# Optimization experiments

Measured on AMD Instinct MI355X. Metric: run time of the kernel, lower is better.

## Reference

```python
import jax, jax.numpy as jnp
import numpy as np

TEMPERATURE = 0.1
SINGLE_POS = False
EPS = 1e-8  # torch CosineSimilarity eps
B, D = 8192, 128
N_DATA = 100000


def setup_inputs() -> dict:
    key = jax.random.key(0)
    k1, k2, k3, k4 = jax.random.split(key, 4)
    features = jax.random.normal(k1, (B, D), dtype=jnp.float32)
    data_ix = jax.random.randint(k2, (B,), 0, N_DATA, dtype=jnp.int64)
    targets_t = jax.random.randint(k3, (N_DATA,), 0, 2, dtype=jnp.int64)
    targets_p = jax.random.randint(k4, (N_DATA,), 0, 2, dtype=jnp.int64)
    return {"features": features, "data_ix": data_ix,
            "targets_t": targets_t, "targets_p": targets_p}


def reference(features, data_ix, targets_t, targets_p):
    tt = targets_t[data_ix]  # [B]
    tp = targets_p[data_ix]  # [B]

    # cosine similarity matrix [B, B] (torch CosineSimilarity semantics)
    norms = jnp.linalg.norm(features, axis=1)  # [B]
    dots = features @ features.T               # [B, B]
    sim = dots / jnp.maximum(norms[:, None] * norms[None, :], EPS)
    logits = sim / TEMPERATURE                 # log(exp(sim/T)) == sim/T
    exp_sim = jnp.exp(logits)

    # pos: same true label, different predicted label; neg: reversed
    same_t = tt[:, None] == tt[None, :]
    same_p = tp[:, None] == tp[None, :]
    pos_mask = same_t & ~same_p   # excludes self automatically
    neg_mask = ~same_t & same_p

    pos_cnt = pos_mask.sum(axis=1)  # [B]
    neg_cnt = neg_mask.sum(axis=1)  # [B]

    exp_pos_sum = jnp.sum(jnp.where(pos_mask, exp_sim, 0.0), axis=1)  # [B]
    exp_neg_sum = jnp.sum(jnp.where(neg_mask, exp_sim, 0.0), axis=1)  # [B]

    if SINGLE_POS:
        # per-pair denominator: log(exp_neg_sum + exp_pos_ij)
        log_denom = jnp.log(exp_neg_sum[:, None] + exp_sim)  # [B, B]
        log_probs_sum = jnp.sum(jnp.where(pos_mask, logits - log_denom, 0.0), axis=1)
    else:
        log_denom = jnp.log(exp_neg_sum + exp_pos_sum)  # [B]
        log_probs_sum = jnp.sum(jnp.where(pos_mask, logits - log_denom[:, None], 0.0), axis=1)

    valid = (pos_cnt > 0) & (neg_cnt > 0)
    mean_log_probs = jnp.where(valid,
                               log_probs_sum / jnp.maximum(pos_cnt, 1).astype(logits.dtype),
                               0.0)
    loss = -jnp.sum(mean_log_probs) / features.shape[0]
    return loss
```

## Files before the change

### kernel.cpp

```cpp
#include <hip/hip_runtime.h>


#define NB 8192
#define ND 128
#define NIB 64
#define JS 16
#define TEMP_INV 10.0f
#define LOG2E 1.4426950408889634f
#define EXPK (TEMP_INV * LOG2E)

typedef __attribute__((ext_vector_type(8))) short short8;
typedef __attribute__((ext_vector_type(4))) float f32x4;

#define OFF_G    0
#define OFF_CLS  (NB * ND * 2)
#define OFF_CNT  (OFF_CLS + NB)
#define OFF_EPP  (OFF_CNT + 64)
#define OFF_ENP  (OFF_EPP + NB * 4 * JS)
#define OFF_LSP  (OFF_ENP + NB * 4 * JS)
#define OFF_CO   OFF_EPP
#define OFF_RL   (OFF_EPP + NB)

__device__ __forceinline__ unsigned short f2bf(float x) {
    unsigned int u = __float_as_uint(x);
    unsigned int r = (u + 0x7FFFu + ((u >> 16) & 1u)) >> 16;
    return (unsigned short)r;
}

__device__ __forceinline__ float fast_exp2(float x) {
#if __has_builtin(__builtin_amdgcn_exp2f)
    return __builtin_amdgcn_exp2f(x);
#else
    return exp2f(x);
#endif
}

__global__ __launch_bounds__(256) void classify_kernel(
    const int* __restrict__ dix, const int* __restrict__ tt, const int* __restrict__ tp,
    unsigned char* __restrict__ clsO, unsigned short* __restrict__ rlocal,
    int* __restrict__ cntP, float* __restrict__ out)
{
    __shared__ int lh[4];
    const int h = blockIdx.x, tid = threadIdx.x;
    if (tid < 4) lh[tid] = 0;
    __syncthreads();
    #pragma unroll
    for (int k = 0; k < 8; ++k) {
        const int row = h * 2048 + k * 256 + tid;
        const int ix  = dix[row];
        const int c   = ((tt[ix] & 1) << 1) | (tp[ix] & 1);
        clsO[row] = (unsigned char)c;
        rlocal[row] = (unsigned short)atomicAdd(&lh[c], 1);
    }
    if (h == 0 && tid == 0) *out = 0.0f;
    __syncthreads();
    if (tid < 4) cntP[h * 4 + tid] = lh[tid];
}

__global__ __launch_bounds__(256) void normscatter_kernel(
    const float* __restrict__ F, const unsigned char* __restrict__ clsO,
    const unsigned short* __restrict__ rlocal, const int* __restrict__ cntP,
    unsigned short* __restrict__ G, unsigned char* __restrict__ clsS)
{
    const int row  = blockIdx.x * 4 + (threadIdx.x >> 6);
    const int lane = threadIdx.x & 63;
    const int c = clsO[row];
    const int h = row >> 11;
    int base = (int)rlocal[row];
    #pragma unroll
    for (int cc = 0; cc < 3; ++cc)
        if (cc < c) base += cntP[cc] + cntP[4 + cc] + cntP[8 + cc] + cntP[12 + cc];
    #pragma unroll
    for (int hh = 0; hh < 3; ++hh)
        if (hh < h) base += cntP[hh * 4 + c];

    const float2 v = *(const float2*)(F + row * ND + lane * 2);
    float ss = v.x * v.x + v.y * v.y;
    #pragma unroll
    for (int m = 1; m < 64; m <<= 1) ss += __shfl_xor(ss, m, 64);
    const float inv = rsqrtf(fmaxf(ss, 1e-24f));
    ushort2 st; st.x = f2bf(v.x * inv); st.y = f2bf(v.y * inv);
    *(ushort2*)(G + base * ND + lane * 2) = st;
    if (lane == 0) clsS[base] = (unsigned char)c;
}

template<bool DOP, bool DON>
__device__ __forceinline__ void seg_tiles(
    const unsigned short* __restrict__ G,
    const short8 (&A)[2][4], unsigned int rcLo, unsigned int rcHi, int s,
    float (&Ep)[8], float (&En)[8], float (&Ls)[8],
    int cs, int ce, int t0, int t1, int l16, int q)
{
    const int s1 = s ^ 1, s2 = s ^ 2;
    float wp[8], wn[8];
    #pragma unroll
    for (int r = 0; r < 4; ++r) {
        const int cLo = (rcLo >> (8 * r)) & 0xff;
        const int cHi = (rcHi >> (8 * r)) & 0xff;
        if (DOP) { wp[r] = (cLo == s1) ? 1.f : 0.f; wp[4 + r] = (cHi == s1) ? 1.f : 0.f; }
        if (DON) { wn[r] = (cLo == s2) ? 1.f : 0.f; wn[4 + r] = (cHi == s2) ? 1.f : 0.f; }
    }
    for (int t = t0; t < t1; ++t) {
        const int j0 = cs + (t << 4);
        int jc = j0 + l16;
        jc = (jc < NB - 1) ? jc : (NB - 1);
        const unsigned short* gj = G + jc * ND + q * 8;
        short8 Bf[4];
        #pragma unroll
        for (int c = 0; c < 4; ++c) Bf[c] = *(const short8*)(gj + c * 32);
        f32x4 acc0 = {0.f, 0.f, 0.f, 0.f}, acc1 = {0.f, 0.f, 0.f, 0.f};
        #pragma unroll
        for (int c = 0; c < 4; ++c)
            acc0 = __builtin_amdgcn_mfma_f32_16x16x32_bf16(A[0][c], Bf[c], acc0, 0, 0, 0);
        #pragma unroll
        for (int c = 0; c < 4; ++c)
            acc1 = __builtin_amdgcn_mfma_f32_16x16x32_bf16(A[1][c], Bf[c], acc1, 0, 0, 0);
        if (j0 + 16 <= ce) {
            #pragma unroll
            for (int r = 0; r < 4; ++r) {
                const float sv0 = acc0[r], sv1 = acc1[r];
                const float e0 = fast_exp2(sv0 * EXPK);
                const float e1 = fast_exp2(sv1 * EXPK);
                if (DOP) {
                    Ep[r]     = fmaf(wp[r],     e0,  Ep[r]);
                    Ls[r]     = fmaf(wp[r],     sv0, Ls[r]);
                    Ep[4 + r] = fmaf(wp[4 + r], e1,  Ep[4 + r]);
                    Ls[4 + r] = fmaf(wp[4 + r], sv1, Ls[4 + r]);
                }
                if (DON) {
                    En[r]     = fmaf(wn[r],     e0, En[r]);
                    En[4 + r] = fmaf(wn[4 + r], e1, En[4 + r]);
                }
            }
        } else {
            const float vm = ((j0 + l16) < ce) ? 1.f : 0.f;
            #pragma unroll
            for (int r = 0; r < 4; ++r) {
                const float sv0 = acc0[r] * vm, sv1 = acc1[r] * vm;
                const float e0 = fast_exp2(sv0 * EXPK) * vm;
                const float e1 = fast_exp2(sv1 * EXPK) * vm;
                if (DOP) {
                    Ep[r]     = fmaf(wp[r],     e0,  Ep[r]);
                    Ls[r]     = fmaf(wp[r],     sv0, Ls[r]);
                    Ep[4 + r] = fmaf(wp[4 + r], e1,  Ep[4 + r]);
                    Ls[4 + r] = fmaf(wp[4 + r], sv1, Ls[4 + r]);
                }
                if (DON) {
                    En[r]     = fmaf(wn[r],     e0, En[r]);
                    En[4 + r] = fmaf(wn[4 + r], e1, En[4 + r]);
                }
            }
        }
    }
}

__global__ __launch_bounds__(256, 4) void sim_kernel(
    const unsigned short* __restrict__ G, const unsigned char* __restrict__ clsS,
    const int* __restrict__ cntP,
    float* __restrict__ EpP, float* __restrict__ EnP, float* __restrict__ LsP)
{
    const int ib = blockIdx.x & (NIB - 1);
    const int jb = blockIdx.x >> 6;
    const int wave = threadIdx.x >> 6, lane = threadIdx.x & 63;
    const int q = lane >> 4, l16 = lane & 15;
    const int ri = ib * 128 + wave * 32;

    short8 A[2][4];
    #pragma unroll
    for (int t = 0; t < 2; ++t)
        #pragma unroll
        for (int c = 0; c < 4; ++c)
            A[t][c] = *(const short8*)(G + (ri + 16 * t + l16) * ND + c * 32 + q * 8);

    const unsigned int rcLo = *(const unsigned int*)(clsS + ri + 4 * q);
    const unsigned int rcHi = *(const unsigned int*)(clsS + ri + 16 + 4 * q);
    const int wF = clsS[ri], wL = clsS[ri + 31];

    float Ep[8], En[8], Ls[8];
    #pragma unroll
    for (int i = 0; i < 8; ++i) { Ep[i] = 0.f; En[i] = 0.f; Ls[i] = 0.f; }

    int cs = 0;
    #pragma unroll 1
    for (int s = 0; s < 4; ++s) {
        const int len = cntP[s] + cntP[4 + s] + cntP[8 + s] + cntP[12 + s];
        const int ce = cs + len;
        const int s1 = s ^ 1, s2 = s ^ 2;
        const bool aP = (s1 >= wF) && (s1 <= wL);
        const bool aN = (s2 >= wF) && (s2 <= wL);
        if (aP || aN) {
            const int nt = (len + 15) >> 4;
            const int t0 = (jb * nt) >> 4;
            const int t1 = ((jb + 1) * nt) >> 4;
            if (aP && aN) seg_tiles<true,  true >(G, A, rcLo, rcHi, s, Ep, En, Ls, cs, ce, t0, t1, l16, q);
            else if (aP)  seg_tiles<true,  false>(G, A, rcLo, rcHi, s, Ep, En, Ls, cs, ce, t0, t1, l16, q);
            else          seg_tiles<false, true >(G, A, rcLo, rcHi, s, Ep, En, Ls, cs, ce, t0, t1, l16, q);
        }
        cs = ce;
    }

    #pragma unroll
    for (int m = 1; m < 16; m <<= 1)
        #pragma unroll
        for (int i = 0; i < 8; ++i) {
            Ep[i] += __shfl_xor(Ep[i], m, 64);
            En[i] += __shfl_xor(En[i], m, 64);
            Ls[i] += __shfl_xor(Ls[i], m, 64);
        }
    if (l16 == 0) {
        #pragma unroll
        for (int t = 0; t < 2; ++t)
            #pragma unroll
            for (int r = 0; r < 4; ++r) {
                const int row = ri + 16 * t + 4 * q + r;
                const int i = t * 4 + r;
                EpP[jb * NB + row] = Ep[i];
                EnP[jb * NB + row] = En[i];
                LsP[jb * NB + row] = Ls[i];
            }
    }
}

__global__ __launch_bounds__(256) void finalize_kernel(
    const float* __restrict__ EpP, const float* __restrict__ EnP,
    const float* __restrict__ LsP, const unsigned char* __restrict__ clsS,
    const int* __restrict__ cntP, float* __restrict__ out)
{
    const int i = blockIdx.x * 256 + threadIdx.x;
    const int tot0 = cntP[0] + cntP[4] + cntP[8]  + cntP[12];
    const int tot1 = cntP[1] + cntP[5] + cntP[9]  + cntP[13];
    const int tot2 = cntP[2] + cntP[6] + cntP[10] + cntP[14];
    const int tot3 = cntP[3] + cntP[7] + cntP[11] + cntP[15];
    const int c = clsS[i];
    const int pc = c ^ 1, nc = c ^ 2;
    const int pcnt = (pc == 0) ? tot0 : (pc == 1) ? tot1 : (pc == 2) ? tot2 : tot3;
    const int ncnt = (nc == 0) ? tot0 : (nc == 1) ? tot1 : (nc == 2) ? tot2 : tot3;
    float ep = 0.f, en = 0.f, ls = 0.f;
    #pragma unroll
    for (int jb = 0; jb < JS; ++jb) {
        ep += EpP[jb * NB + i];
        en += EnP[jb * NB + i];
        ls += LsP[jb * NB + i];
    }
    float contrib = 0.0f;
    if (pcnt > 0 && ncnt > 0) {
        const float ld = logf(ep + en);
        contrib = -(TEMP_INV * ls - (float)pcnt * ld) / ((float)pcnt * (float)NB);
    }
    #pragma unroll
    for (int m = 1; m < 64; m <<= 1) contrib += __shfl_xor(contrib, m, 64);
    __shared__ float wsum[4];
    if ((threadIdx.x & 63) == 0) wsum[threadIdx.x >> 6] = contrib;
    __syncthreads();
    if (threadIdx.x == 0)
        atomicAdd(out, wsum[0] + wsum[1] + wsum[2] + wsum[3]);
}

extern "C" void kernel_launch(void* const* d_in, const int* in_sizes, int n_in,
                              void* d_out, int out_size, void* d_ws, size_t ws_size,
                              hipStream_t stream) {
    const float* F = (const float*)d_in[0];
    const int* dix = (const int*)d_in[1];
    const int* tt  = (const int*)d_in[2];
    const int* tp  = (const int*)d_in[3];
    float* out = (float*)d_out;

    char* ws = (char*)d_ws;
    unsigned short* G   = (unsigned short*)(ws + OFF_G);
    unsigned char* clsS = (unsigned char*)(ws + OFF_CLS);
    int* cntP           = (int*)(ws + OFF_CNT);
    float* EpP          = (float*)(ws + OFF_EPP);
    float* EnP          = (float*)(ws + OFF_ENP);
    float* LsP          = (float*)(ws + OFF_LSP);
    unsigned char* clsO = (unsigned char*)(ws + OFF_CO);
    unsigned short* rl  = (unsigned short*)(ws + OFF_RL);

    classify_kernel<<<4, 256, 0, stream>>>(dix, tt, tp, clsO, rl, cntP, out);
    normscatter_kernel<<<2048, 256, 0, stream>>>(F, clsO, rl, cntP, G, clsS);
    sim_kernel<<<NIB * JS, 256, 0, stream>>>(G, clsS, cntP, EpP, EnP, LsP);
    finalize_kernel<<<NB / 256, 256, 0, stream>>>(EpP, EnP, LsP, clsS, cntP, out);
}
```

Measured before the change: 119.7 us.

## Stage B tiles cooperatively in shared memory with register-prefetched double buffering

Each 16-row B tile was previously loaded from global memory separately by every wave. Now the four waves load it together into a double-buffered LDS tile, and the next tile is prefetched into registers, so global traffic per block drops about fourfold and loads overlap with MFMA work. In exchange the activity test moves from per-wave to per-block class ranges, extra barriers are added per tile, and waves with no work still have to join the barrier loop.

```diff
diff --git a/kernel.cpp b/kernel.cpp
--- a/kernel.cpp
+++ b/kernel.cpp
@@ -11,6 +11,7 @@
 
 typedef __attribute__((ext_vector_type(8))) short short8;
 typedef __attribute__((ext_vector_type(4))) float f32x4;
+typedef __attribute__((ext_vector_type(4))) unsigned int u32x4;
 
 #define OFF_G    0
 #define OFF_CLS  (NB * ND * 2)
@@ -84,86 +85,19 @@
     if (lane == 0) clsS[base] = (unsigned char)c;
 }
 
-template<bool DOP, bool DON>
-__device__ __forceinline__ void seg_tiles(
-    const unsigned short* __restrict__ G,
-    const short8 (&A)[2][4], unsigned int rcLo, unsigned int rcHi, int s,
-    float (&Ep)[8], float (&En)[8], float (&Ls)[8],
-    int cs, int ce, int t0, int t1, int l16, int q)
-{
-    const int s1 = s ^ 1, s2 = s ^ 2;
-    float wp[8], wn[8];
-    #pragma unroll
-    for (int r = 0; r < 4; ++r) {
-        const int cLo = (rcLo >> (8 * r)) & 0xff;
-        const int cHi = (rcHi >> (8 * r)) & 0xff;
-        if (DOP) { wp[r] = (cLo == s1) ? 1.f : 0.f; wp[4 + r] = (cHi == s1) ? 1.f : 0.f; }
-        if (DON) { wn[r] = (cLo == s2) ? 1.f : 0.f; wn[4 + r] = (cHi == s2) ? 1.f : 0.f; }
-    }
-    for (int t = t0; t < t1; ++t) {
-        const int j0 = cs + (t << 4);
-        int jc = j0 + l16;
-        jc = (jc < NB - 1) ? jc : (NB - 1);
-        const unsigned short* gj = G + jc * ND + q * 8;
-        short8 Bf[4];
-        #pragma unroll
-        for (int c = 0; c < 4; ++c) Bf[c] = *(const short8*)(gj + c * 32);
-        f32x4 acc0 = {0.f, 0.f, 0.f, 0.f}, acc1 = {0.f, 0.f, 0.f, 0.f};
-        #pragma unroll
-        for (int c = 0; c < 4; ++c)
-            acc0 = __builtin_amdgcn_mfma_f32_16x16x32_bf16(A[0][c], Bf[c], acc0, 0, 0, 0);
-        #pragma unroll
-        for (int c = 0; c < 4; ++c)
-            acc1 = __builtin_amdgcn_mfma_f32_16x16x32_bf16(A[1][c], Bf[c], acc1, 0, 0, 0);
-        if (j0 + 16 <= ce) {
-            #pragma unroll
-            for (int r = 0; r < 4; ++r) {
-                const float sv0 = acc0[r], sv1 = acc1[r];
-                const float e0 = fast_exp2(sv0 * EXPK);
-                const float e1 = fast_exp2(sv1 * EXPK);
-                if (DOP) {
-                    Ep[r]     = fmaf(wp[r],     e0,  Ep[r]);
-                    Ls[r]     = fmaf(wp[r],     sv0, Ls[r]);
-                    Ep[4 + r] = fmaf(wp[4 + r], e1,  Ep[4 + r]);
-                    Ls[4 + r] = fmaf(wp[4 + r], sv1, Ls[4 + r]);
-                }
-                if (DON) {
-                    En[r]     = fmaf(wn[r],     e0, En[r]);
-                    En[4 + r] = fmaf(wn[4 + r], e1, En[4 + r]);
-                }
-            }
-        } else {
-            const float vm = ((j0 + l16) < ce) ? 1.f : 0.f;
-            #pragma unroll
-            for (int r = 0; r < 4; ++r) {
-                const float sv0 = acc0[r] * vm, sv1 = acc1[r] * vm;
-                const float e0 = fast_exp2(sv0 * EXPK) * vm;
-                const float e1 = fast_exp2(sv1 * EXPK) * vm;
-                if (DOP) {
-                    Ep[r]     = fmaf(wp[r],     e0,  Ep[r]);
-                    Ls[r]     = fmaf(wp[r],     sv0, Ls[r]);
-                    Ep[4 + r] = fmaf(wp[4 + r], e1,  Ep[4 + r]);
-                    Ls[4 + r] = fmaf(wp[4 + r], sv1, Ls[4 + r]);
-                }
-                if (DON) {
-                    En[r]     = fmaf(wn[r],     e0, En[r]);
-                    En[4 + r] = fmaf(wn[4 + r], e1, En[4 + r]);
-                }
-            }
-        }
-    }
-}
-
 __global__ __launch_bounds__(256, 4) void sim_kernel(
     const unsigned short* __restrict__ G, const unsigned char* __restrict__ clsS,
     const int* __restrict__ cntP,
     float* __restrict__ EpP, float* __restrict__ EnP, float* __restrict__ LsP)
 {
+    __shared__ __align__(16) unsigned short Bt[2][16][136];
+
     const int ib = blockIdx.x & (NIB - 1);
     const int jb = blockIdx.x >> 6;
     const int wave = threadIdx.x >> 6, lane = threadIdx.x & 63;
     const int q = lane >> 4, l16 = lane & 15;
     const int ri = ib * 128 + wave * 32;
+    const int wr = wave << 2;
 
     short8 A[2][4];
     #pragma unroll
@@ -175,10 +109,13 @@
     const unsigned int rcLo = *(const unsigned int*)(clsS + ri + 4 * q);
     const unsigned int rcHi = *(const unsigned int*)(clsS + ri + 16 + 4 * q);
     const int wF = clsS[ri], wL = clsS[ri + 31];
+    const int bF = clsS[ib * 128], bL = clsS[ib * 128 + 127];
 
     float Ep[8], En[8], Ls[8];
     #pragma unroll
     for (int i = 0; i < 8; ++i) { Ep[i] = 0.f; En[i] = 0.f; Ls[i] = 0.f; }
+
+    const u32x4* G4 = (const u32x4*)G;
 
     int cs = 0;
     #pragma unroll 1
@@ -186,15 +123,107 @@
         const int len = cntP[s] + cntP[4 + s] + cntP[8 + s] + cntP[12 + s];
         const int ce = cs + len;
         const int s1 = s ^ 1, s2 = s ^ 2;
-        const bool aP = (s1 >= wF) && (s1 <= wL);
-        const bool aN = (s2 >= wF) && (s2 <= wL);
+        const bool aP = (s1 >= bF) && (s1 <= bL);
+        const bool aN = (s2 >= bF) && (s2 <= bL);
         if (aP || aN) {
             const int nt = (len + 15) >> 4;
             const int t0 = (jb * nt) >> 4;
             const int t1 = ((jb + 1) * nt) >> 4;
-            if (aP && aN) seg_tiles<true,  true >(G, A, rcLo, rcHi, s, Ep, En, Ls, cs, ce, t0, t1, l16, q);
-            else if (aP)  seg_tiles<true,  false>(G, A, rcLo, rcHi, s, Ep, En, Ls, cs, ce, t0, t1, l16, q);
-            else          seg_tiles<false, true >(G, A, rcLo, rcHi, s, Ep, En, Ls, cs, ce, t0, t1, l16, q);
+            if (t0 < t1) {
+                float wp[8], wn[8];
+                #pragma unroll
+                for (int r = 0; r < 4; ++r) {
+                    const int cLo = (rcLo >> (8 * r)) & 0xff;
+                    const int cHi = (rcHi >> (8 * r)) & 0xff;
+                    wp[r]     = (cLo == s1) ? 1.f : 0.f;
+                    wp[4 + r] = (cHi == s1) ? 1.f : 0.f;
+                    wn[r]     = (cLo == s2) ? 1.f : 0.f;
+                    wn[4 + r] = (cHi == s2) ? 1.f : 0.f;
+                }
+                const bool aPw = (s1 >= wF) && (s1 <= wL);
+                const bool aNw = (s2 >= wF) && (s2 <= wL);
+
+                u32x4 st;
+                {
+                    int rw = cs + (t0 << 4) + wr + (lane >> 4);
+                    rw = (rw < NB - 1) ? rw : (NB - 1);
+                    st = G4[rw * 16 + (lane & 15)];
+                    *(u32x4*)&Bt[0][wr + (lane >> 4)][(lane & 15) * 8] = st;
+                }
+                if (t0 + 1 < t1) {
+                    int rw = cs + ((t0 + 1) << 4) + wr + (lane >> 4);
+                    rw = (rw < NB - 1) ? rw : (NB - 1);
+                    st = G4[rw * 16 + (lane & 15)];
+                }
+                asm volatile("s_waitcnt lgkmcnt(0)" ::: "memory");
+                asm volatile("s_barrier" ::: "memory");
+
+                #pragma unroll 1
+                for (int t = t0; t < t1; ++t) {
+                    const int buf = (t - t0) & 1;
+                    const int j0 = cs + (t << 4);
+                    if (aPw || aNw) {
+                        short8 Bf[4];
+                        #pragma unroll
+                        for (int c = 0; c < 4; ++c)
+                            Bf[c] = *(const short8*)&Bt[buf][l16][c * 32 + q * 8];
+                        f32x4 acc0 = {0.f, 0.f, 0.f, 0.f}, acc1 = {0.f, 0.f, 0.f, 0.f};
+                        #pragma unroll
+                        for (int c = 0; c < 4; ++c)
+                            acc0 = __builtin_amdgcn_mfma_f32_16x16x32_bf16(A[0][c], Bf[c], acc0, 0, 0, 0);
+                        #pragma unroll
+                        for (int c = 0; c < 4; ++c)
+                            acc1 = __builtin_amdgcn_mfma_f32_16x16x32_bf16(A[1][c], Bf[c], acc1, 0, 0, 0);
+                        if (j0 + 16 <= ce) {
+                            #pragma unroll
+                            for (int r = 0; r < 4; ++r) {
+                                const float sv0 = acc0[r], sv1 = acc1[r];
+                                const float e0 = fast_exp2(sv0 * EXPK);
+                                const float e1 = fast_exp2(sv1 * EXPK);
+                                if (aPw) {
+                                    Ep[r]     = fmaf(wp[r],     e0,  Ep[r]);
+                                    Ls[r]     = fmaf(wp[r],     sv0, Ls[r]);
+                                    Ep[4 + r] = fmaf(wp[4 + r], e1,  Ep[4 + r]);
+                                    Ls[4 + r] = fmaf(wp[4 + r], sv1, Ls[4 + r]);
+                                }
+                                if (aNw) {
+                                    En[r]     = fmaf(wn[r],     e0, En[r]);
+                                    En[4 + r] = fmaf(wn[4 + r], e1, En[4 + r]);
+                                }
+                            }
+                        } else {
+                            const float vm = ((j0 + l16) < ce) ? 1.f : 0.f;
+                            #pragma unroll
+                            for (int r = 0; r < 4; ++r) {
+                                const float sv0 = acc0[r] * vm, sv1 = acc1[r] * vm;
+                                const float e0 = fast_exp2(sv0 * EXPK) * vm;
+                                const float e1 = fast_exp2(sv1 * EXPK) * vm;
+                                if (aPw) {
+                                    Ep[r]     = fmaf(wp[r],     e0,  Ep[r]);
+                                    Ls[r]     = fmaf(wp[r],     sv0, Ls[r]);
+                                    Ep[4 + r] = fmaf(wp[4 + r], e1,  Ep[4 + r]);
+                                    Ls[4 + r] = fmaf(wp[4 + r], sv1, Ls[4 + r]);
+                                }
+                                if (aNw) {
+                                    En[r]     = fmaf(wn[r],     e0, En[r]);
+                                    En[4 + r] = fmaf(wn[4 + r], e1, En[4 + r]);
+                                }
+                            }
+                        }
+                    }
+                    asm volatile("s_barrier" ::: "memory");
+                    if (t + 1 < t1) {
+                        *(u32x4*)&Bt[buf ^ 1][wr + (lane >> 4)][(lane & 15) * 8] = st;
+                        if (t + 2 < t1) {
+                            int rw = cs + ((t + 2) << 4) + wr + (lane >> 4);
+                            rw = (rw < NB - 1) ? rw : (NB - 1);
+                            st = G4[rw * 16 + (lane & 15)];
+                        }
+                        asm volatile("s_waitcnt lgkmcnt(0)" ::: "memory");
+                        asm volatile("s_barrier" ::: "memory");
+                    }
+                }
+            }
         }
         cs = ce;
     }
```

Result: faster. 116.5 us (-2.7%).

## Stage B tiles in LDS via async global_load_lds with double buffering

Applied to the files above, without the earlier changes.

Each wave used to load its own B fragments from global memory for every 16-column tile. Now the block cooperatively stages 64-row B panels into a double-buffered LDS array with global_load_lds, using a rotated chunk layout to avoid bank conflicts, so the four waves share each load. The next panel's load overlaps the current MFMA/exp work. The cost is block-level barriers and a coarser 64-row work split, and waves with no active segment still wait at the syncs.

```diff
diff --git a/kernel.cpp b/kernel.cpp
--- a/kernel.cpp
+++ b/kernel.cpp
@@ -33,6 +33,12 @@
 #else
     return exp2f(x);
 #endif
+}
+
+typedef const __attribute__((address_space(1))) void gas_void;
+typedef __attribute__((address_space(3))) void las_void;
+__device__ __forceinline__ void gload_lds16(const void* g, void* s) {
+    __builtin_amdgcn_global_load_lds((gas_void*)g, (las_void*)s, 16, 0, 0);
 }
 
 __global__ __launch_bounds__(256) void classify_kernel(
@@ -84,86 +90,21 @@
     if (lane == 0) clsS[base] = (unsigned char)c;
 }
 
-template<bool DOP, bool DON>
-__device__ __forceinline__ void seg_tiles(
-    const unsigned short* __restrict__ G,
-    const short8 (&A)[2][4], unsigned int rcLo, unsigned int rcHi, int s,
-    float (&Ep)[8], float (&En)[8], float (&Ls)[8],
-    int cs, int ce, int t0, int t1, int l16, int q)
-{
-    const int s1 = s ^ 1, s2 = s ^ 2;
-    float wp[8], wn[8];
-    #pragma unroll
-    for (int r = 0; r < 4; ++r) {
-        const int cLo = (rcLo >> (8 * r)) & 0xff;
-        const int cHi = (rcHi >> (8 * r)) & 0xff;
-        if (DOP) { wp[r] = (cLo == s1) ? 1.f : 0.f; wp[4 + r] = (cHi == s1) ? 1.f : 0.f; }
-        if (DON) { wn[r] = (cLo == s2) ? 1.f : 0.f; wn[4 + r] = (cHi == s2) ? 1.f : 0.f; }
-    }
-    for (int t = t0; t < t1; ++t) {
-        const int j0 = cs + (t << 4);
-        int jc = j0 + l16;
-        jc = (jc < NB - 1) ? jc : (NB - 1);
-        const unsigned short* gj = G + jc * ND + q * 8;
-        short8 Bf[4];
-        #pragma unroll
-        for (int c = 0; c < 4; ++c) Bf[c] = *(const short8*)(gj + c * 32);
-        f32x4 acc0 = {0.f, 0.f, 0.f, 0.f}, acc1 = {0.f, 0.f, 0.f, 0.f};
-        #pragma unroll
-        for (int c = 0; c < 4; ++c)
-            acc0 = __builtin_amdgcn_mfma_f32_16x16x32_bf16(A[0][c], Bf[c], acc0, 0, 0, 0);
-        #pragma unroll
-        for (int c = 0; c < 4; ++c)
-            acc1 = __builtin_amdgcn_mfma_f32_16x16x32_bf16(A[1][c], Bf[c], acc1, 0, 0, 0);
-        if (j0 + 16 <= ce) {
-            #pragma unroll
-            for (int r = 0; r < 4; ++r) {
-                const float sv0 = acc0[r], sv1 = acc1[r];
-                const float e0 = fast_exp2(sv0 * EXPK);
-                const float e1 = fast_exp2(sv1 * EXPK);
-                if (DOP) {
-                    Ep[r]     = fmaf(wp[r],     e0,  Ep[r]);
-                    Ls[r]     = fmaf(wp[r],     sv0, Ls[r]);
-                    Ep[4 + r] = fmaf(wp[4 + r], e1,  Ep[4 + r]);
-                    Ls[4 + r] = fmaf(wp[4 + r], sv1, Ls[4 + r]);
-                }
-                if (DON) {
-                    En[r]     = fmaf(wn[r],     e0, En[r]);
-                    En[4 + r] = fmaf(wn[4 + r], e1, En[4 + r]);
-                }
-            }
-        } else {
-            const float vm = ((j0 + l16) < ce) ? 1.f : 0.f;
-            #pragma unroll
-            for (int r = 0; r < 4; ++r) {
-                const float sv0 = acc0[r] * vm, sv1 = acc1[r] * vm;
-                const float e0 = fast_exp2(sv0 * EXPK) * vm;
-                const float e1 = fast_exp2(sv1 * EXPK) * vm;
-                if (DOP) {
-                    Ep[r]     = fmaf(wp[r],     e0,  Ep[r]);
-                    Ls[r]     = fmaf(wp[r],     sv0, Ls[r]);
-                    Ep[4 + r] = fmaf(wp[4 + r], e1,  Ep[4 + r]);
-                    Ls[4 + r] = fmaf(wp[4 + r], sv1, Ls[4 + r]);
-                }
-                if (DON) {
-                    En[r]     = fmaf(wn[r],     e0, En[r]);
-                    En[4 + r] = fmaf(wn[4 + r], e1, En[4 + r]);
-                }
-            }
-        }
-    }
-}
-
 __global__ __launch_bounds__(256, 4) void sim_kernel(
     const unsigned short* __restrict__ G, const unsigned char* __restrict__ clsS,
     const int* __restrict__ cntP,
     float* __restrict__ EpP, float* __restrict__ EnP, float* __restrict__ LsP)
 {
+    __shared__ unsigned short Blds[2][64 * 128];
+
     const int ib = blockIdx.x & (NIB - 1);
     const int jb = blockIdx.x >> 6;
     const int wave = threadIdx.x >> 6, lane = threadIdx.x & 63;
     const int q = lane >> 4, l16 = lane & 15;
     const int ri = ib * 128 + wave * 32;
+    const int wu = __builtin_amdgcn_readfirstlane(wave);
+    const int lrow4 = lane >> 4;
+    const int lpos  = lane & 15;
 
     short8 A[2][4];
     #pragma unroll
@@ -175,6 +116,7 @@
     const unsigned int rcLo = *(const unsigned int*)(clsS + ri + 4 * q);
     const unsigned int rcHi = *(const unsigned int*)(clsS + ri + 16 + 4 * q);
     const int wF = clsS[ri], wL = clsS[ri + 31];
+    const int bF = clsS[ib * 128], bL = clsS[ib * 128 + 127];
 
     float Ep[8], En[8], Ls[8];
     #pragma unroll
@@ -186,15 +128,97 @@
         const int len = cntP[s] + cntP[4 + s] + cntP[8 + s] + cntP[12 + s];
         const int ce = cs + len;
         const int s1 = s ^ 1, s2 = s ^ 2;
-        const bool aP = (s1 >= wF) && (s1 <= wL);
-        const bool aN = (s2 >= wF) && (s2 <= wL);
-        if (aP || aN) {
-            const int nt = (len + 15) >> 4;
-            const int t0 = (jb * nt) >> 4;
-            const int t1 = ((jb + 1) * nt) >> 4;
-            if (aP && aN) seg_tiles<true,  true >(G, A, rcLo, rcHi, s, Ep, En, Ls, cs, ce, t0, t1, l16, q);
-            else if (aP)  seg_tiles<true,  false>(G, A, rcLo, rcHi, s, Ep, En, Ls, cs, ce, t0, t1, l16, q);
-            else          seg_tiles<false, true >(G, A, rcLo, rcHi, s, Ep, En, Ls, cs, ce, t0, t1, l16, q);
+        const bool aPb = (s1 >= bF) && (s1 <= bL);
+        const bool aNb = (s2 >= bF) && (s2 <= bL);
+        if (aPb || aNb) {
+            const int np = (len + 63) >> 6;
+            const int p0 = (jb * np) >> 4;
+            const int p1 = ((jb + 1) * np) >> 4;
+            if (p0 < p1) {
+                float wp[8], wn[8];
+                #pragma unroll
+                for (int r = 0; r < 4; ++r) {
+                    const int cLo = (rcLo >> (8 * r)) & 0xff;
+                    const int cHi = (rcHi >> (8 * r)) & 0xff;
+                    wp[r]     = (cLo == s1) ? 1.f : 0.f;
+                    wp[4 + r] = (cHi == s1) ? 1.f : 0.f;
+                    wn[r]     = (cLo == s2) ? 1.f : 0.f;
+                    wn[4 + r] = (cHi == s2) ? 1.f : 0.f;
+                }
+                const bool act = ((s1 >= wF) && (s1 <= wL)) ||
+                                 ((s2 >= wF) && (s2 <= wL));
+
+                #define STAGE(BUF, P)                                              \
+                    _Pragma("unroll")                                              \
+                    for (int j = 0; j < 4; ++j) {                                  \
+                        const int pr = wu * 16 + j * 4 + lrow4;                    \
+                        int rowG = cs + (P) * 64 + pr;                             \
+                        rowG = (rowG < NB - 1) ? rowG : (NB - 1);                  \
+                        const int chunk = (lpos - pr) & 15;                        \
+                        gload_lds16(G + rowG * ND + chunk * 8,                     \
+                                    &Blds[BUF][(wu * 16 + j * 4) * ND]);           \
+                    }
+
+                STAGE(0, p0)
+                __syncthreads();
+
+                #pragma unroll 1
+                for (int p = p0; p < p1; ++p) {
+                    const int cur = (p - p0) & 1;
+                    if (p + 1 < p1) STAGE(cur ^ 1, p + 1)
+                    if (act) {
+                        #pragma unroll
+                        for (int st = 0; st < 4; ++st) {
+                            const int j0 = cs + p * 64 + st * 16;
+                            if (j0 >= ce) break;
+                            short8 Bf[4];
+                            #pragma unroll
+                            for (int c = 0; c < 4; ++c) {
+                                const int slot = (c * 4 + q + l16) & 15;
+                                Bf[c] = *(const short8*)
+                                    &Blds[cur][(st * 16 + l16) * ND + slot * 8];
+                            }
+                            f32x4 acc0 = {0.f, 0.f, 0.f, 0.f}, acc1 = {0.f, 0.f, 0.f, 0.f};
+                            #pragma unroll
+                            for (int c = 0; c < 4; ++c)
+                                acc0 = __builtin_amdgcn_mfma_f32_16x16x32_bf16(A[0][c], Bf[c], acc0, 0, 0, 0);
+                            #pragma unroll
+                            for (int c = 0; c < 4; ++c)
+                                acc1 = __builtin_amdgcn_mfma_f32_16x16x32_bf16(A[1][c], Bf[c], acc1, 0, 0, 0);
+                            if (j0 + 16 <= ce) {
+                                #pragma unroll
+                                for (int r = 0; r < 4; ++r) {
+                                    const float sv0 = acc0[r], sv1 = acc1[r];
+                                    const float e0 = fast_exp2(sv0 * EXPK);
+                                    const float e1 = fast_exp2(sv1 * EXPK);
+                                    Ep[r]     = fmaf(wp[r],     e0,  Ep[r]);
+                                    Ls[r]     = fmaf(wp[r],     sv0, Ls[r]);
+                                    Ep[4 + r] = fmaf(wp[4 + r], e1,  Ep[4 + r]);
+                                    Ls[4 + r] = fmaf(wp[4 + r], sv1, Ls[4 + r]);
+                                    En[r]     = fmaf(wn[r],     e0, En[r]);
+                                    En[4 + r] = fmaf(wn[4 + r], e1, En[4 + r]);
+                                }
+                            } else {
+                                const float vm = ((j0 + l16) < ce) ? 1.f : 0.f;
+                                #pragma unroll
+                                for (int r = 0; r < 4; ++r) {
+                                    const float sv0 = acc0[r] * vm, sv1 = acc1[r] * vm;
+                                    const float e0 = fast_exp2(sv0 * EXPK) * vm;
+                                    const float e1 = fast_exp2(sv1 * EXPK) * vm;
+                                    Ep[r]     = fmaf(wp[r],     e0,  Ep[r]);
+                                    Ls[r]     = fmaf(wp[r],     sv0, Ls[r]);
+                                    Ep[4 + r] = fmaf(wp[4 + r], e1,  Ep[4 + r]);
+                                    Ls[4 + r] = fmaf(wp[4 + r], sv1, Ls[4 + r]);
+                                    En[r]     = fmaf(wn[r],     e0, En[r]);
+                                    En[4 + r] = fmaf(wn[4 + r], e1, En[4 + r]);
+                                }
+                            }
+                        }
+                    }
+                    __syncthreads();
+                }
+                #undef STAGE
+            }
         }
         cs = ce;
     }
```

Result: slower. 124.4 us (+3.9%).
